# Kernel tuning notes

Measured on AMD Instinct MI355X. Metric: run time of the kernel, lower is better.

The kernel has to match this reference:

```python
import jax, jax.numpy as jnp
import numpy as np

D_MODEL = 1024
NUM_HEADS = 16
D_K = D_MODEL // NUM_HEADS
ROPE_BASE = 10000.0


def _rotate_half(x):
    # interleaved pairs: (x0, x1) -> (-x1, x0)
    x1 = x[..., ::2]
    x2 = x[..., 1::2]
    return jnp.stack((-x2, x1), axis=-1).reshape(x.shape)


def _rope(q, k):
    seq_len = q.shape[-2]
    freqs = ROPE_BASE ** (jnp.arange(0, D_K, 2, dtype=q.dtype) / D_K)  # [D_K/2]
    angles = jnp.arange(seq_len, dtype=q.dtype)[:, None] / freqs[None, :]  # [S, D_K/2]
    sin = jnp.repeat(jnp.sin(angles), 2, axis=-1)[None, None]  # [1,1,S,D_K]
    cos = jnp.repeat(jnp.cos(angles), 2, axis=-1)[None, None]
    return q * cos + _rotate_half(q) * sin, k * cos + _rotate_half(k) * sin


def setup_inputs() -> dict:
    key = jax.random.key(0)
    ks = jax.random.split(key, 9)
    B, S, D = 2, 2048, D_MODEL
    s = 1.0 / np.sqrt(D)
    inp = {
        "x": jax.random.normal(ks[0], (B, S, D), dtype=jnp.float32),
        "wq": jax.random.uniform(ks[1], (D, D), jnp.float32, -s, s),
        "bq": jax.random.uniform(ks[2], (D,), jnp.float32, -s, s),
        "wk": jax.random.uniform(ks[3], (D, D), jnp.float32, -s, s),
        "bk": jax.random.uniform(ks[4], (D,), jnp.float32, -s, s),
        "wv": jax.random.uniform(ks[5], (D, D), jnp.float32, -s, s),
        "bv": jax.random.uniform(ks[6], (D,), jnp.float32, -s, s),
        "wo": jax.random.uniform(ks[7], (D, D), jnp.float32, -s, s),
        "bo": jax.random.uniform(ks[8], (D,), jnp.float32, -s, s),
    }
    return inp


def reference(x, wq, bq, wk, bk, wv, bv, wo, bo):
    B, S, D = x.shape
    H, dk = NUM_HEADS, D_K
    # torch Linear: y = x @ W.T + b
    Q = (x @ wq.T + bq).reshape(B, S, H, dk).transpose(0, 2, 1, 3)  # [B,H,S,dk]
    K = (x @ wk.T + bk).reshape(B, S, H, dk).transpose(0, 2, 1, 3)
    V = (x @ wv.T + bv).reshape(B, S, H, dk).transpose(0, 2, 1, 3)
    Q, K = _rope(Q, K)
    score = jnp.einsum("bhqd,bhkd->bhqk", Q, K) / jnp.sqrt(jnp.asarray(dk, x.dtype))
    attn_w = jax.nn.softmax(score, axis=-1)
    out = jnp.einsum("bhqk,bhkd->bhqd", attn_w, V)  # [B,H,S,dk]
    out = out.transpose(0, 2, 1, 3).reshape(B, S, D)
    return out @ wo.T + bo
```

## Files before the change

### kernel.cpp

```cpp
#include <hip/hip_runtime.h>
#include <hip/hip_bf16.h>
#include <math.h>

typedef __bf16 bf16_t;
typedef __bf16 bf16x4_t __attribute__((ext_vector_type(4)));
typedef __bf16 bf16x8_t __attribute__((ext_vector_type(8)));
typedef float  f32x4_t  __attribute__((ext_vector_type(4)));

#define SEQ 2048
#define DM  1024
#define NH  16
#define DK  64
#define ROPE_C 0.4152410118609203f
#define EXP_C (1.4426950408889634f / 8.0f)

#define GLD16(gp, lp) \
  __builtin_amdgcn_global_load_lds((__attribute__((address_space(1))) const void*)(gp), \
                                   (__attribute__((address_space(3))) void*)(lp), 16, 0, 0)

__global__ __launch_bounds__(256)
void prep_kernel(const float* __restrict__ x,  const float* __restrict__ wq,
                 const float* __restrict__ wk, const float* __restrict__ wv,
                 const float* __restrict__ wo, bf16_t* __restrict__ dst,
                 float2* __restrict__ lut) {
  if (blockIdx.x < 8192) {
    int i = blockIdx.x * 256 + threadIdx.x;
    const float* s;
    if (i < 1048576) {
      s = x + (size_t)i * 4;
    } else {
      int j = i - 1048576;
      int w = j >> 18;
      const float* base = (w == 0) ? wq : (w == 1) ? wk : (w == 2) ? wv : wo;
      s = base + (size_t)(j & 262143) * 4;
    }
    float4 v = *(const float4*)s;
    bf16x4_t o;
    o.x = (bf16_t)v.x; o.y = (bf16_t)v.y; o.z = (bf16_t)v.z; o.w = (bf16_t)v.w;
    ((bf16x4_t*)dst)[i] = o;
  } else {
    int i = (blockIdx.x - 8192) * 256 + threadIdx.x;
    int s = i >> 5, f = i & 31;
    float ang = (float)s * exp2f(-ROPE_C * (float)f);
    float sn, cs;
    sincosf(ang, &sn, &cs);
    lut[i] = make_float2(sn, cs);
  }
}

__global__ __launch_bounds__(256)
void gemm_qkv(const bf16_t* __restrict__ A, const bf16_t* __restrict__ Wq,
              const bf16_t* __restrict__ Wk, const bf16_t* __restrict__ Wv,
              const float* __restrict__ bq, const float* __restrict__ bk,
              const float* __restrict__ bv, const float2* __restrict__ lut,
              bf16_t* __restrict__ Qb, bf16_t* __restrict__ Kb,
              bf16_t* __restrict__ Vtb) {
  const int K = 1024;
  __shared__ bf16_t As[128 * 32];
  __shared__ bf16_t Bs[128 * 32];

  const int tid  = threadIdx.x;
  const int w    = tid >> 6;
  const int lane = tid & 63;
  const int quad = lane >> 4;
  const int lrow = lane & 15;
  const int srow = lane >> 2;
  const int scol = (lane & 3) * 8;

  if (blockIdx.x < 512) {
    const int wm = (w >> 1) * 64, wn = (w & 1) * 64;
    const int bm = blockIdx.x >> 4;
    const int bn = blockIdx.x & 15;

    const int isK = bn >> 3;
    const int bnl = bn & 7;
    const bf16_t* Ablk = A + (size_t)(bm * 128) * K;
    const bf16_t* Bblk = (isK ? Wk : Wq) + (size_t)(bnl * 128) * K;
    const float*  bias = isK ? bk : bq;
    bf16_t* D = isK ? Kb : Qb;

    f32x4_t acc[4][4] = {};

    for (int k0 = 0; k0 < K; k0 += 32) {
      GLD16(&Ablk[(size_t)(w * 32 + srow) * K + k0 + scol],      &As[(w * 32) * 32]);
      GLD16(&Ablk[(size_t)(w * 32 + 16 + srow) * K + k0 + scol], &As[(w * 32 + 16) * 32]);
      GLD16(&Bblk[(size_t)(w * 32 + srow) * K + k0 + scol],      &Bs[(w * 32) * 32]);
      GLD16(&Bblk[(size_t)(w * 32 + 16 + srow) * K + k0 + scol], &Bs[(w * 32 + 16) * 32]);
      __syncthreads();

      bf16x8_t af[4], bf[4];
#pragma unroll
      for (int mi = 0; mi < 4; mi++)
        af[mi] = *(const bf16x8_t*)(&As[(wm + mi * 16 + lrow) * 32 + quad * 8]);
#pragma unroll
      for (int ni = 0; ni < 4; ni++)
        bf[ni] = *(const bf16x8_t*)(&Bs[(wn + ni * 16 + lrow) * 32 + quad * 8]);
#pragma unroll
      for (int mi = 0; mi < 4; mi++)
#pragma unroll
        for (int ni = 0; ni < 4; ni++)
          acc[mi][ni] = __builtin_amdgcn_mfma_f32_16x16x32_bf16(af[mi], bf[ni], acc[mi][ni], 0, 0, 0);
      __syncthreads();
    }

    const int brow = bm * 128 + wm;
    const int cbase = bnl * 128 + wn;

#pragma unroll
    for (int ni = 0; ni < 4; ni++) {
      const int col = cbase + ni * 16 + lrow;
      const float bvv = bias[col];
      const int t = col & 63;
      const int h = col >> 6;
      const int fidx = t >> 1;
#pragma unroll
      for (int mi = 0; mi < 4; mi++) {
        f32x4_t v = acc[mi][ni];
#pragma unroll
        for (int r = 0; r < 4; r++) {
          const int row = brow + mi * 16 + quad * 4 + r;
          const int s = row & (SEQ - 1);
          float val = v[r] + bvv;
          const float2 sc = lut[s * 32 + fidx];
          const float pv = __shfl_xor(val, 1);
          val = (t & 1) ? (val * sc.y + pv * sc.x) : (val * sc.y - pv * sc.x);
          const int b = row >> 11;
          const size_t o = (((size_t)(b * NH + h) * SEQ) + s) * DK + t;
          D[o] = (bf16_t)val;
        }
      }
    }
  } else {
    const int j = blockIdx.x - 512;
    const int wm = (w >> 1) * 32, wn = (w & 1) * 64;
    const int bm = j >> 5;
    const int bn = j & 31;

    const bf16_t* Ablk = Wv + (size_t)(bm * 64) * K;
    const bf16_t* Bblk = A  + (size_t)(bn * 128) * K;

    f32x4_t acc[2][4] = {};

    for (int k0 = 0; k0 < K; k0 += 32) {
      GLD16(&Ablk[(size_t)(w * 16 + srow) * K + k0 + scol],      &As[(w * 16) * 32]);
      GLD16(&Bblk[(size_t)(w * 32 + srow) * K + k0 + scol],      &Bs[(w * 32) * 32]);
      GLD16(&Bblk[(size_t)(w * 32 + 16 + srow) * K + k0 + scol], &Bs[(w * 32 + 16) * 32]);
      __syncthreads();

      bf16x8_t af[2], bf[4];
#pragma unroll
      for (int mi = 0; mi < 2; mi++)
        af[mi] = *(const bf16x8_t*)(&As[(wm + mi * 16 + lrow) * 32 + quad * 8]);
#pragma unroll
      for (int ni = 0; ni < 4; ni++)
        bf[ni] = *(const bf16x8_t*)(&Bs[(wn + ni * 16 + lrow) * 32 + quad * 8]);
#pragma unroll
      for (int mi = 0; mi < 2; mi++)
#pragma unroll
        for (int ni = 0; ni < 4; ni++)
          acc[mi][ni] = __builtin_amdgcn_mfma_f32_16x16x32_bf16(af[mi], bf[ni], acc[mi][ni], 0, 0, 0);
      __syncthreads();
    }

    const int fbase = bm * 64 + wm;
    const int tbase = bn * 128 + wn;

#pragma unroll
    for (int ni = 0; ni < 4; ni++) {
      const int t = tbase + ni * 16 + lrow;
      const int b = t >> 11;
      const int s = t & (SEQ - 1);
#pragma unroll
      for (int mi = 0; mi < 2; mi++) {
        f32x4_t v = acc[mi][ni];
        const int f = fbase + mi * 16 + quad * 4;
        const int h = f >> 6, d = f & 63;
#pragma unroll
        for (int r = 0; r < 4; r++)
          Vtb[((size_t)((b * NH + h) * DK + d + r)) * SEQ + s] = (bf16_t)(v[r] + bv[f + r]);
      }
    }
  }
}

__global__ __launch_bounds__(256)
void gemm_out(const bf16_t* __restrict__ A, const bf16_t* __restrict__ Bw,
              const float* __restrict__ bias, float* __restrict__ D) {
  const int K = 1024;
  __shared__ bf16_t As[128 * 32];
  __shared__ bf16_t Bs[64 * 32];

  const int tid  = threadIdx.x;
  const int w    = tid >> 6;
  const int lane = tid & 63;
  const int quad = lane >> 4;
  const int lrow = lane & 15;
  const int wm = (w >> 1) * 64, wn = (w & 1) * 32;
  const int bm = blockIdx.y, bn = blockIdx.x;

  const bf16_t* Ablk = A  + (size_t)(bm * 128) * K;
  const bf16_t* Bblk = Bw + (size_t)(bn * 64) * K;

  f32x4_t acc[4][2] = {};

  const int srow = lane >> 2;
  const int scol = (lane & 3) * 8;

  for (int k0 = 0; k0 < K; k0 += 32) {
    GLD16(&Ablk[(size_t)(w * 32 + srow) * K + k0 + scol],      &As[(w * 32) * 32]);
    GLD16(&Ablk[(size_t)(w * 32 + 16 + srow) * K + k0 + scol], &As[(w * 32 + 16) * 32]);
    GLD16(&Bblk[(size_t)(w * 16 + srow) * K + k0 + scol],      &Bs[(w * 16) * 32]);
    __syncthreads();

    bf16x8_t af[4], bf[2];
#pragma unroll
    for (int mi = 0; mi < 4; mi++)
      af[mi] = *(const bf16x8_t*)(&As[(wm + mi * 16 + lrow) * 32 + quad * 8]);
#pragma unroll
    for (int ni = 0; ni < 2; ni++)
      bf[ni] = *(const bf16x8_t*)(&Bs[(wn + ni * 16 + lrow) * 32 + quad * 8]);
#pragma unroll
    for (int mi = 0; mi < 4; mi++)
#pragma unroll
      for (int ni = 0; ni < 2; ni++)
        acc[mi][ni] = __builtin_amdgcn_mfma_f32_16x16x32_bf16(af[mi], bf[ni], acc[mi][ni], 0, 0, 0);
    __syncthreads();
  }

#pragma unroll
  for (int ni = 0; ni < 2; ni++) {
    const int col = bn * 64 + wn + ni * 16 + lrow;
    const float bvv = bias[col];
#pragma unroll
    for (int mi = 0; mi < 4; mi++) {
      f32x4_t v = acc[mi][ni];
#pragma unroll
      for (int r = 0; r < 4; r++) {
        const int row = bm * 128 + wm + mi * 16 + quad * 4 + r;
        D[(size_t)row * DM + col] = v[r] + bvv;
      }
    }
  }
}

__global__ __launch_bounds__(512)
void attn_kernel(const bf16_t* __restrict__ Q, const bf16_t* __restrict__ K,
                 const bf16_t* __restrict__ Vt, bf16_t* __restrict__ AO) {
  __shared__ bf16_t Ks[128 * 72];
  __shared__ bf16_t Vs[64 * 136];

  const int tid  = threadIdx.x;
  const int w    = tid >> 6;
  const int lane = tid & 63;
  const int quad = lane >> 4;
  const int lrow = lane & 15;
  const int bh = blockIdx.y;
  const int q0 = blockIdx.x * 128 + w * 16;

  const bf16_t* Qh  = Q  + (size_t)bh * SEQ * DK;
  const bf16_t* Kh  = K  + (size_t)bh * SEQ * DK;
  const bf16_t* Vth = Vt + (size_t)bh * DK * SEQ;

  bf16x8_t qf[2];
#pragma unroll
  for (int c = 0; c < 2; c++) {
    bf16x8_t t = *(const bf16x8_t*)(&Qh[(size_t)(q0 + lrow) * DK + c * 32 + quad * 8]);
#pragma unroll
    for (int i = 0; i < 8; i++) t[i] = (bf16_t)((float)t[i] * EXP_C);
    qf[c] = t;
  }

  f32x4_t accO[4] = {};
  float lsum = 0.f;

  const int krow = tid >> 2;
  const int kcol = (tid & 3) * 16;
  const int vrow = tid >> 3;
  const int vcol = (tid & 7) * 16;

  uint4 kr0 = *(const uint4*)(&Kh[(size_t)krow * DK + kcol]);
  uint4 kr1 = *(const uint4*)(&Kh[(size_t)krow * DK + kcol + 8]);
  uint4 vr0 = *(const uint4*)(&Vth[(size_t)vrow * SEQ + vcol]);
  uint4 vr1 = *(const uint4*)(&Vth[(size_t)vrow * SEQ + vcol + 8]);

  for (int kt = 0; kt < SEQ / 128; ++kt) {
    *(uint4*)(&Ks[krow * 72 + kcol])      = kr0;
    *(uint4*)(&Ks[krow * 72 + kcol + 8])  = kr1;
    *(uint4*)(&Vs[vrow * 136 + vcol])     = vr0;
    *(uint4*)(&Vs[vrow * 136 + vcol + 8]) = vr1;
    __syncthreads();

    if (kt + 1 < SEQ / 128) {
      const int kb = (kt + 1) * 128;
      kr0 = *(const uint4*)(&Kh[(size_t)(kb + krow) * DK + kcol]);
      kr1 = *(const uint4*)(&Kh[(size_t)(kb + krow) * DK + kcol + 8]);
      vr0 = *(const uint4*)(&Vth[(size_t)vrow * SEQ + kb + vcol]);
      vr1 = *(const uint4*)(&Vth[(size_t)vrow * SEQ + kb + vcol + 8]);
    }

#pragma unroll
    for (int c2 = 0; c2 < 4; ++c2) {
      uint2 pk[2];
#pragma unroll
      for (int kk2 = 0; kk2 < 2; ++kk2) {
        const int kk = c2 * 2 + kk2;
        bf16x8_t kf0 = *(const bf16x8_t*)(&Ks[(kk * 16 + lrow) * 72 + quad * 8]);
        bf16x8_t kf1 = *(const bf16x8_t*)(&Ks[(kk * 16 + lrow) * 72 + 32 + quad * 8]);
        f32x4_t z = {};
        z = __builtin_amdgcn_mfma_f32_16x16x32_bf16(kf0, qf[0], z, 0, 0, 0);
        z = __builtin_amdgcn_mfma_f32_16x16x32_bf16(kf1, qf[1], z, 0, 0, 0);
        const float p0 = __builtin_amdgcn_exp2f(z[0]), p1 = __builtin_amdgcn_exp2f(z[1]);
        const float p2 = __builtin_amdgcn_exp2f(z[2]), p3 = __builtin_amdgcn_exp2f(z[3]);
        lsum += (p0 + p1) + (p2 + p3);
        pk[kk2].x = __builtin_amdgcn_perm(__builtin_bit_cast(unsigned, p1),
                                          __builtin_bit_cast(unsigned, p0), 0x07060302u);
        pk[kk2].y = __builtin_amdgcn_perm(__builtin_bit_cast(unsigned, p3),
                                          __builtin_bit_cast(unsigned, p2), 0x07060302u);
      }
      uint4 pfu;
      pfu.x = pk[0].x; pfu.y = pk[0].y; pfu.z = pk[1].x; pfu.w = pk[1].y;
      bf16x8_t pf = __builtin_bit_cast(bf16x8_t, pfu);
#pragma unroll
      for (int nt = 0; nt < 4; ++nt) {
        const bf16_t* vbase = &Vs[(nt * 16 + lrow) * 136 + c2 * 32 + quad * 4];
        bf16x8_t vf;
        *(bf16x4_t*)(&vf)       = *(const bf16x4_t*)(vbase);
        *((bf16x4_t*)(&vf) + 1) = *(const bf16x4_t*)(vbase + 16);
        accO[nt] = __builtin_amdgcn_mfma_f32_16x16x32_bf16(pf, vf, accO[nt], 0, 0, 0);
      }
    }
    __syncthreads();
  }

  lsum += __shfl_xor(lsum, 16);
  lsum += __shfl_xor(lsum, 32);
  float linv[4];
#pragma unroll
  for (int r = 0; r < 4; r++)
    linv[r] = 1.0f / __shfl(lsum, quad * 4 + r);

  const int b = bh >> 4, h = bh & 15;
#pragma unroll
  for (int nt = 0; nt < 4; nt++)
#pragma unroll
    for (int r = 0; r < 4; r++) {
      const int srowq = q0 + quad * 4 + r;
      const float val = accO[nt][r] * linv[r];
      const size_t o = ((size_t)(b * SEQ + srowq)) * DM + h * DK + nt * 16 + lrow;
      AO[o] = (bf16_t)val;
    }
}

extern "C" void kernel_launch(void* const* d_in, const int* in_sizes, int n_in,
                              void* d_out, int out_size, void* d_ws, size_t ws_size,
                              hipStream_t stream) {
  const float* x  = (const float*)d_in[0];
  const float* wq = (const float*)d_in[1];
  const float* bq = (const float*)d_in[2];
  const float* wk = (const float*)d_in[3];
  const float* bk = (const float*)d_in[4];
  const float* wv = (const float*)d_in[5];
  const float* bv = (const float*)d_in[6];
  const float* wo = (const float*)d_in[7];
  const float* bo = (const float*)d_in[8];
  float* out = (float*)d_out;

  char* ws = (char*)d_ws;
  bf16_t* xb   = (bf16_t*)(ws);
  bf16_t* wqb  = (bf16_t*)(ws + 8388608);
  bf16_t* wkb  = (bf16_t*)(ws + 10485760);
  bf16_t* wvb  = (bf16_t*)(ws + 12582912);
  bf16_t* wob  = (bf16_t*)(ws + 14680064);
  bf16_t* Qb   = (bf16_t*)(ws + 16777216);
  bf16_t* Kb   = (bf16_t*)(ws + 25165824);
  bf16_t* Vtb  = (bf16_t*)(ws + 33554432);
  bf16_t* AOb  = (bf16_t*)(ws + 41943040);
  float2* lut  = (float2*)(ws + 50331648);

  prep_kernel<<<8448, 256, 0, stream>>>(x, wq, wk, wv, wo, xb, lut);

  gemm_qkv<<<1024, 256, 0, stream>>>(xb, wqb, wkb, wvb, bq, bk, bv, lut, Qb, Kb, Vtb);

  attn_kernel<<<dim3(SEQ / 128, 2 * NH), 512, 0, stream>>>(Qb, Kb, Vtb, AOb);

  gemm_out<<<dim3(16, 32), 256, 0, stream>>>(AOb, wob, bo, out);
}
```

Before: 211.5 us.

## Swizzle block order for XCD locality and double attention KV tile size

```diff
diff --git a/kernel.cpp b/kernel.cpp
--- a/kernel.cpp
+++ b/kernel.cpp
@@ -67,10 +67,13 @@
   const int srow = lane >> 2;
   const int scol = (lane & 3) * 8;
 
-  if (blockIdx.x < 512) {
+  const int id  = blockIdx.x;
+  const int swz = (id & 7) * 128 + (id >> 3);
+
+  if (swz < 512) {
     const int wm = (w >> 1) * 64, wn = (w & 1) * 64;
-    const int bm = blockIdx.x >> 4;
-    const int bn = blockIdx.x & 15;
+    const int bm = swz >> 4;
+    const int bn = swz & 15;
 
     const int isK = bn >> 3;
     const int bnl = bn & 7;
@@ -131,7 +134,7 @@
       }
     }
   } else {
-    const int j = blockIdx.x - 512;
+    const int j = swz - 512;
     const int wm = (w >> 1) * 32, wn = (w & 1) * 64;
     const int bm = j >> 5;
     const int bn = j & 31;
@@ -196,7 +199,11 @@
   const int quad = lane >> 4;
   const int lrow = lane & 15;
   const int wm = (w >> 1) * 64, wn = (w & 1) * 32;
-  const int bm = blockIdx.y, bn = blockIdx.x;
+
+  const int id  = blockIdx.x;
+  const int swz = (id & 7) * 64 + (id >> 3);
+  const int bm  = swz >> 4;
+  const int bn  = swz & 15;
 
   const bf16_t* Ablk = A  + (size_t)(bm * 128) * K;
   const bf16_t* Bblk = Bw + (size_t)(bn * 64) * K;
@@ -246,16 +253,19 @@
 __global__ __launch_bounds__(512)
 void attn_kernel(const bf16_t* __restrict__ Q, const bf16_t* __restrict__ K,
                  const bf16_t* __restrict__ Vt, bf16_t* __restrict__ AO) {
-  __shared__ bf16_t Ks[128 * 72];
-  __shared__ bf16_t Vs[64 * 136];
+  __shared__ bf16_t Ks[256 * 72];
+  __shared__ bf16_t Vs[64 * 264];
 
   const int tid  = threadIdx.x;
   const int w    = tid >> 6;
   const int lane = tid & 63;
   const int quad = lane >> 4;
   const int lrow = lane & 15;
-  const int bh = blockIdx.y;
-  const int q0 = blockIdx.x * 128 + w * 16;
+
+  const int id  = blockIdx.x;
+  const int swz = (id & 7) * 64 + (id >> 3);
+  const int bh  = swz >> 4;
+  const int q0  = (swz & 15) * 128 + w * 16;
 
   const bf16_t* Qh  = Q  + (size_t)bh * SEQ * DK;
   const bf16_t* Kh  = K  + (size_t)bh * SEQ * DK;
@@ -273,33 +283,38 @@
   f32x4_t accO[4] = {};
   float lsum = 0.f;
 
-  const int krow = tid >> 2;
-  const int kcol = (tid & 3) * 16;
-  const int vrow = tid >> 3;
-  const int vcol = (tid & 7) * 16;
-
-  uint4 kr0 = *(const uint4*)(&Kh[(size_t)krow * DK + kcol]);
-  uint4 kr1 = *(const uint4*)(&Kh[(size_t)krow * DK + kcol + 8]);
-  uint4 vr0 = *(const uint4*)(&Vth[(size_t)vrow * SEQ + vcol]);
-  uint4 vr1 = *(const uint4*)(&Vth[(size_t)vrow * SEQ + vcol + 8]);
-
-  for (int kt = 0; kt < SEQ / 128; ++kt) {
-    *(uint4*)(&Ks[krow * 72 + kcol])      = kr0;
-    *(uint4*)(&Ks[krow * 72 + kcol + 8])  = kr1;
-    *(uint4*)(&Vs[vrow * 136 + vcol])     = vr0;
-    *(uint4*)(&Vs[vrow * 136 + vcol + 8]) = vr1;
+  const int krA = tid >> 3;
+  const int kcA = (tid & 7) * 8;
+  const int vrA = tid >> 5;
+  const int vcA = (tid & 31) * 8;
+
+  uint4 kr[4], vr[4];
+#pragma unroll
+  for (int i = 0; i < 4; i++) {
+    kr[i] = *(const uint4*)(&Kh[(size_t)(krA + 64 * i) * DK + kcA]);
+    vr[i] = *(const uint4*)(&Vth[(size_t)(vrA + 16 * i) * SEQ + vcA]);
+  }
+
+  for (int kt = 0; kt < SEQ / 256; ++kt) {
+#pragma unroll
+    for (int i = 0; i < 4; i++) {
+      *(uint4*)(&Ks[(krA + 64 * i) * 72 + kcA])  = kr[i];
+      *(uint4*)(&Vs[(vrA + 16 * i) * 264 + vcA]) = vr[i];
+    }
     __syncthreads();
 
-    if (kt + 1 < SEQ / 128) {
-      const int kb = (kt + 1) * 128;
-      kr0 = *(const uint4*)(&Kh[(size_t)(kb + krow) * DK + kcol]);
-      kr1 = *(const uint4*)(&Kh[(size_t)(kb + krow) * DK + kcol + 8]);
-      vr0 = *(const uint4*)(&Vth[(size_t)vrow * SEQ + kb + vcol]);
-      vr1 = *(const uint4*)(&Vth[(size_t)vrow * SEQ + kb + vcol + 8]);
-    }
-
-#pragma unroll
-    for (int c2 = 0; c2 < 4; ++c2) {
+    if (kt + 1 < SEQ / 256) {
+      const int kb = (kt + 1) * 256;
+#pragma unroll
+      for (int i = 0; i < 4; i++) {
+        kr[i] = *(const uint4*)(&Kh[(size_t)(kb + krA + 64 * i) * DK + kcA]);
+        vr[i] = *(const uint4*)(&Vth[(size_t)(vrA + 16 * i) * SEQ + kb + vcA]);
+      }
+    }
+
+    __builtin_amdgcn_s_setprio(1);
+#pragma unroll
+    for (int c2 = 0; c2 < 8; ++c2) {
       uint2 pk[2];
 #pragma unroll
       for (int kk2 = 0; kk2 < 2; ++kk2) {
@@ -322,13 +337,14 @@
       bf16x8_t pf = __builtin_bit_cast(bf16x8_t, pfu);
 #pragma unroll
       for (int nt = 0; nt < 4; ++nt) {
-        const bf16_t* vbase = &Vs[(nt * 16 + lrow) * 136 + c2 * 32 + quad * 4];
+        const bf16_t* vbase = &Vs[(nt * 16 + lrow) * 264 + c2 * 32 + quad * 4];
         bf16x8_t vf;
         *(bf16x4_t*)(&vf)       = *(const bf16x4_t*)(vbase);
         *((bf16x4_t*)(&vf) + 1) = *(const bf16x4_t*)(vbase + 16);
         accO[nt] = __builtin_amdgcn_mfma_f32_16x16x32_bf16(pf, vf, accO[nt], 0, 0, 0);
       }
     }
+    __builtin_amdgcn_s_setprio(0);
     __syncthreads();
   }
 
@@ -381,7 +397,7 @@
 
   gemm_qkv<<<1024, 256, 0, stream>>>(xb, wqb, wkb, wvb, bq, bk, bv, lut, Qb, Kb, Vtb);
 
-  attn_kernel<<<dim3(SEQ / 128, 2 * NH), 512, 0, stream>>>(Qb, Kb, Vtb, AOb);
-
-  gemm_out<<<dim3(16, 32), 256, 0, stream>>>(AOb, wob, bo, out);
+  attn_kernel<<<512, 512, 0, stream>>>(Qb, Kb, Vtb, AOb);
+
+  gemm_out<<<512, 256, 0, stream>>>(AOb, wob, bo, out);
 }
```

Result: slower. 268.2 us (+26.8%).
